# Optimization experiments

Measured on AMD Instinct MI355X. Metric: run time of the kernel, lower is better.

## Reference

```python
import jax, jax.numpy as jnp
import numpy as np

B, S, E, H = 64, 512, 768, 256


def setup_inputs() -> dict:
    key = jax.random.key(0)
    ks = jax.random.split(key, 9)
    sc = 0.02  # small init so relu-activated LSTM stays numerically sane
    x = jax.random.normal(ks[0], (B, S, E), dtype=jnp.float32)
    kernel_f = jax.random.normal(ks[1], (E, 4 * H), dtype=jnp.float32) * sc
    rec_f = jax.random.normal(ks[2], (H, 4 * H), dtype=jnp.float32) * sc
    bias_f = jnp.zeros((4 * H,), dtype=jnp.float32)
    kernel_b = jax.random.normal(ks[3], (E, 4 * H), dtype=jnp.float32) * sc
    rec_b = jax.random.normal(ks[4], (H, 4 * H), dtype=jnp.float32) * sc
    bias_b = jnp.zeros((4 * H,), dtype=jnp.float32)
    Wd = jax.random.normal(ks[5], (S * H, 2), dtype=jnp.float32) * sc
    bd = jnp.zeros((2,), dtype=jnp.float32)
    return {"x": x, "kernel_f": kernel_f, "rec_f": rec_f, "bias_f": bias_f,
            "kernel_b": kernel_b, "rec_b": rec_b, "bias_b": bias_b,
            "Wd": Wd, "bd": bd}


def _lstm_relu(x, kernel, rec, bias):
    # Keras LSTM with activation='relu', recurrent_activation='sigmoid'.
    # Gate order in keras kernel: [i, f, c, o].
    b, h = x.shape[0], rec.shape[0]
    xz = jnp.einsum('bse,eg->bsg', x, kernel) + bias  # [B,S,4H] precomputed input part

    def step(carry, zt):
        hp, cp = carry
        z = zt + hp @ rec  # [B,4H]
        zi, zf, zc, zo = jnp.split(z, 4, axis=-1)
        i = jax.nn.sigmoid(zi)
        f = jax.nn.sigmoid(zf)
        o = jax.nn.sigmoid(zo)
        c = f * cp + i * jax.nn.relu(zc)
        hn = o * jax.nn.relu(c)
        return (hn, c), hn

    init = (jnp.zeros((b, h), x.dtype), jnp.zeros((b, h), x.dtype))
    _, hs = jax.lax.scan(step, init, jnp.swapaxes(xz, 0, 1))  # [S,B,H]
    return jnp.swapaxes(hs, 0, 1)  # [B,S,H]


def reference(x, kernel_f, rec_f, bias_f, kernel_b, rec_b, bias_b, Wd, bd):
    h_fwd = _lstm_relu(x, kernel_f, rec_f, bias_f)
    # backward direction: process reversed sequence, reverse output back, then merge_mode='sum'
    h_bwd = _lstm_relu(x[:, ::-1], kernel_b, rec_b, bias_b)[:, ::-1]
    h = h_fwd + h_bwd  # [B,S,H]
    # dropout is identity at inference (training=None)
    flat = h.reshape(h.shape[0], -1)  # [B, S*H]
    logits = flat @ Wd + bd  # [B,2]
    return logits
```

## Files before the change

kernel.cpp:

```cpp
#include <hip/hip_runtime.h>
#include <hip/hip_bf16.h>
#include <hip/hip_fp16.h>

#define B_ 64
#define S_ 512
#define E_ 768
#define H_ 256
#define G_ 1024
#define MROWS 32768

typedef float f32x4 __attribute__((ext_vector_type(4)));
typedef float f32x16 __attribute__((ext_vector_type(16)));
typedef short short8 __attribute__((ext_vector_type(8)));
typedef _Float16 v2h __attribute__((ext_vector_type(2)));
typedef unsigned int u32x4 __attribute__((ext_vector_type(4)));


__global__ void cast_x_kernel(const float* __restrict__ x, __hip_bfloat16* __restrict__ xbf, int n) {
    int i = (blockIdx.x * 256 + threadIdx.x) * 4;
    if (i >= n) return;
    float4 v = *(const float4*)(x + i);
    xbf[i + 0] = __float2bfloat16(v.x);
    xbf[i + 1] = __float2bfloat16(v.y);
    xbf[i + 2] = __float2bfloat16(v.z);
    xbf[i + 3] = __float2bfloat16(v.w);
}

__global__ void prep_kT_kernel(const float* __restrict__ kf, const float* __restrict__ kb,
                               __hip_bfloat16* __restrict__ kT) {
    int idx = blockIdx.x * 256 + threadIdx.x;
    int dir = blockIdx.y;
    const float* src = dir ? kb : kf;
    int k = idx >> 10;
    int n = idx & 1023;
    float v = src[idx];
    kT[(size_t)dir * G_ * E_ + (size_t)n * E_ + k] = __float2bfloat16(v);
}

__global__ void prep_recQ_kernel(const float* __restrict__ rf, const float* __restrict__ rb,
                                 unsigned int* __restrict__ recQ) {
    int idx = blockIdx.x * 256 + threadIdx.x;
    int dir = blockIdx.y;
    const float* src = dir ? rb : rf;
    int g  = idx & 1023;
    int u  = (idx >> 10) & 3;
    int kk = idx >> 12;
    int k0 = 8 * kk + 2 * u;
    float a = src[(size_t)k0 * G_ + g];
    float b = src[(size_t)(k0 + 1) * G_ + g];
    v2h p;
    p[0] = (_Float16)a;
    p[1] = (_Float16)b;
    recQ[(size_t)dir * 131072 + (size_t)kk * 4096 + g * 4 + u] = __builtin_bit_cast(unsigned int, p);
}

#define TM 128
#define TN 128
#define BK 32
#define LDA 40

__global__ __launch_bounds__(256) void gemm_xz_kernel(
        const __hip_bfloat16* __restrict__ xbf,
        const __hip_bfloat16* __restrict__ kT,
        const float* __restrict__ bias_f, const float* __restrict__ bias_b,
        __hip_bfloat16* __restrict__ xz) {
    int dir  = blockIdx.z;
    int nblk = blockIdx.x;
    int mblk = blockIdx.y;
    int tid  = threadIdx.x;
    int wave = tid >> 6, lane = tid & 63;

    __shared__ __hip_bfloat16 shA[TM * LDA];
    __shared__ __hip_bfloat16 shB[TN * LDA];

    int m0 = mblk * TM;
    int n0 = nblk * TN;

    int rowl0 = tid >> 2;
    int rowl1 = rowl0 + 64;
    int k8    = (tid & 3) * 8;
    int ar0 = m0 + rowl0, ar1 = m0 + rowl1;
    int sa0 = (ar0 & ~511) | (dir ? (511 - (ar0 & 511)) : (ar0 & 511));
    int sa1 = (ar1 & ~511) | (dir ? (511 - (ar1 & 511)) : (ar1 & 511));
    const __hip_bfloat16* kbase = kT + (size_t)dir * G_ * E_;

    f32x16 acc[4] = {};

    int lm = lane & 31;
    int kq = (lane >> 5) * 8;

    for (int k0 = 0; k0 < E_; k0 += BK) {
        __syncthreads();
        *(short8*)&shA[rowl0 * LDA + k8] = *(const short8*)(xbf + (size_t)sa0 * E_ + k0 + k8);
        *(short8*)&shA[rowl1 * LDA + k8] = *(const short8*)(xbf + (size_t)sa1 * E_ + k0 + k8);
        *(short8*)&shB[rowl0 * LDA + k8] = *(const short8*)(kbase + (size_t)(n0 + rowl0) * E_ + k0 + k8);
        *(short8*)&shB[rowl1 * LDA + k8] = *(const short8*)(kbase + (size_t)(n0 + rowl1) * E_ + k0 + k8);
        __syncthreads();

#pragma unroll
        for (int kk = 0; kk < BK; kk += 16) {
            short8 afrag = *(const short8*)&shA[(wave * 32 + lm) * LDA + kk + kq];
#pragma unroll
            for (int j = 0; j < 4; ++j) {
                short8 bfrag = *(const short8*)&shB[(j * 32 + lm) * LDA + kk + kq];
                acc[j] = __builtin_amdgcn_mfma_f32_32x32x16_bf16(afrag, bfrag, acc[j], 0, 0, 0);
            }
        }
    }

    const float* bias = dir ? bias_b : bias_f;
#pragma unroll
    for (int j = 0; j < 4; ++j) {
        int col = n0 + j * 32 + lm;
        float bv = bias[col];
#pragma unroll
        for (int reg = 0; reg < 16; ++reg) {
            int row = m0 + wave * 32 + (reg & 3) + 8 * (reg >> 2) + 4 * (lane >> 5);
            xz[((size_t)dir * MROWS + row) * G_ + col] = __float2bfloat16(acc[j][reg] + bv);
        }
    }
}

__device__ inline float dot2f16(unsigned int rbits, unsigned int hbits, float acc) {
#if __has_builtin(__builtin_amdgcn_fdot2)
    return __builtin_amdgcn_fdot2(__builtin_bit_cast(v2h, rbits),
                                  __builtin_bit_cast(v2h, hbits), acc, false);
#else
    v2h r = __builtin_bit_cast(v2h, rbits);
    v2h h = __builtin_bit_cast(v2h, hbits);
    return acc + (float)r[0] * (float)h[0] + (float)r[1] * (float)h[1];
#endif
}

__device__ inline float sigmoidf(float x) { return 1.f / (1.f + __expf(-x)); }

#define KKREG 24
#define KKLDS 8
__global__ __launch_bounds__(512) void scan_kernel(
        const __hip_bfloat16* __restrict__ xz,
        const uint4* __restrict__ recQ,
        const float* __restrict__ Wd,
        const float* __restrict__ bd,
        float* __restrict__ out) {
    int b = blockIdx.x, dir = blockIdx.y, tid = threadIdx.x;
    __shared__ __align__(16) uint4 sh_rec[KKLDS * G_];
    __shared__ __align__(16) _Float16 sh_h[2][H_];
    __shared__ float sh_z[G_];
    __shared__ float rbuf[8];

    const uint4* rqbase = recQ + (size_t)dir * 32768;

    u32x4 rr0[KKREG], rr1[KKREG];
    {
        unsigned long long a0 = (unsigned long long)(const void*)(rqbase + tid);
        unsigned long long a1 = (unsigned long long)(const void*)(rqbase + tid + 512);
#pragma unroll
        for (int kk = 0; kk < KKREG; ++kk) {
            unsigned long long ka0 = a0 + (unsigned long long)kk * 16384ull;
            unsigned long long ka1 = a1 + (unsigned long long)kk * 16384ull;
            asm volatile("global_load_dwordx4 %0, %1, off" : "=v"(rr0[kk]) : "v"(ka0));
            asm volatile("global_load_dwordx4 %0, %1, off" : "=v"(rr1[kk]) : "v"(ka1));
        }
        asm volatile("s_waitcnt vmcnt(0)" ::: "memory");
    }

#pragma unroll
    for (int j = 0; j < KKLDS * 2; ++j)
        sh_rec[j * 512 + tid] = rqbase[KKREG * 1024 + j * 512 + tid];

    if (tid < H_) { sh_h[0][tid] = (_Float16)0.f; }
    float c = 0.f, pl0 = 0.f, pl1 = 0.f;
    const __hip_bfloat16* xzb = xz + ((size_t)dir * MROWS + (size_t)b * S_) * G_ + tid;
    __syncthreads();

    int p = 0;
    for (int s = 0; s < S_; ++s) {
        float xz0 = __bfloat162float(xzb[(size_t)s * G_]);
        float xz1 = __bfloat162float(xzb[(size_t)s * G_ + 512]);
        float2 wv = {0.f, 0.f};
        int t = dir ? (S_ - 1 - s) : s;
        if (tid < H_) wv = ((const float2*)Wd)[t * H_ + tid];

        const uint4* hp = (const uint4*)&sh_h[p][0];
        float z0a = 0.f, z0b = 0.f, z1a = 0.f, z1b = 0.f;

#pragma unroll
        for (int kk = 0; kk < KKREG; ++kk) {
            uint4 hv = hp[kk];
            u32x4 r0 = rr0[kk];
            u32x4 r1 = rr1[kk];
            z0a = dot2f16(r0.x, hv.x, z0a); z0b = dot2f16(r0.y, hv.y, z0b);
            z0a = dot2f16(r0.z, hv.z, z0a); z0b = dot2f16(r0.w, hv.w, z0b);
            z1a = dot2f16(r1.x, hv.x, z1a); z1b = dot2f16(r1.y, hv.y, z1b);
            z1a = dot2f16(r1.z, hv.z, z1a); z1b = dot2f16(r1.w, hv.w, z1b);
        }
#pragma unroll
        for (int j = 0; j < KKLDS; ++j) {
            uint4 hv = hp[KKREG + j];
            uint4 r0 = sh_rec[j * 1024 + tid];
            uint4 r1 = sh_rec[j * 1024 + tid + 512];
            z0a = dot2f16(r0.x, hv.x, z0a); z0b = dot2f16(r0.y, hv.y, z0b);
            z0a = dot2f16(r0.z, hv.z, z0a); z0b = dot2f16(r0.w, hv.w, z0b);
            z1a = dot2f16(r1.x, hv.x, z1a); z1b = dot2f16(r1.y, hv.y, z1b);
            z1a = dot2f16(r1.z, hv.z, z1a); z1b = dot2f16(r1.w, hv.w, z1b);
        }
        sh_z[tid]       = z0a + z0b + xz0;
        sh_z[tid + 512] = z1a + z1b + xz1;
        __syncthreads();

        if (tid < H_) {
            float zi = sh_z[tid];
            float zf = sh_z[H_ + tid];
            float zc = sh_z[2 * H_ + tid];
            float zo = sh_z[3 * H_ + tid];
            float ig = sigmoidf(zi);
            float fg = sigmoidf(zf);
            float og = sigmoidf(zo);
            float cc = fmaxf(zc, 0.f);
            c = fg * c + ig * cc;
            float h = og * fmaxf(c, 0.f);
            sh_h[p ^ 1][tid] = (_Float16)h;

            pl0 = fmaf(h, wv.x, pl0);
            pl1 = fmaf(h, wv.y, pl1);
        }
        __syncthreads();
        p ^= 1;
    }

    if (tid < H_) {
#pragma unroll
        for (int off = 32; off > 0; off >>= 1) {
            pl0 += __shfl_down(pl0, off);
            pl1 += __shfl_down(pl1, off);
        }
    }
    if (tid < H_ && (tid & 63) == 0) {
        int w = tid >> 6;
        rbuf[w] = pl0; rbuf[4 + w] = pl1;
    }
    __syncthreads();
    if (tid == 0) {
        float t0 = rbuf[0] + rbuf[1] + rbuf[2] + rbuf[3];
        float t1 = rbuf[4] + rbuf[5] + rbuf[6] + rbuf[7];
        atomicAdd(&out[b * 2 + 0], t0);
        atomicAdd(&out[b * 2 + 1], t1);
    }
    if (dir == 0 && tid < 2) atomicAdd(&out[b * 2 + tid], bd[tid]);
}

extern "C" void kernel_launch(void* const* d_in, const int* in_sizes, int n_in,
                              void* d_out, int out_size, void* d_ws, size_t ws_size,
                              hipStream_t stream) {
    const float* x        = (const float*)d_in[0];
    const float* kernel_f = (const float*)d_in[1];
    const float* rec_f    = (const float*)d_in[2];
    const float* bias_f   = (const float*)d_in[3];
    const float* kernel_b = (const float*)d_in[4];
    const float* rec_b    = (const float*)d_in[5];
    const float* bias_b   = (const float*)d_in[6];
    const float* Wd       = (const float*)d_in[7];
    const float* bd       = (const float*)d_in[8];
    float* out = (float*)d_out;

    char* w = (char*)d_ws;
    __hip_bfloat16* xz  = (__hip_bfloat16*)w;
    __hip_bfloat16* xbf = (__hip_bfloat16*)(w + 134217728);
    __hip_bfloat16* kT  = (__hip_bfloat16*)(w + 184549376);
    unsigned int*  recQ = (unsigned int*) (w + 187695104);

    int nx = B_ * S_ * E_;
    cast_x_kernel<<<nx / (256 * 4), 256, 0, stream>>>(x, xbf, nx);
    prep_kT_kernel<<<dim3((E_ * G_) / 256, 2), 256, 0, stream>>>(kernel_f, kernel_b, kT);
    prep_recQ_kernel<<<dim3(131072 / 256, 2), 256, 0, stream>>>(rec_f, rec_b, recQ);

    gemm_xz_kernel<<<dim3(G_ / TN, MROWS / TM, 2), 256, 0, stream>>>(xbf, kT, bias_f, bias_b, xz);

    hipMemsetAsync(d_out, 0, (size_t)out_size * sizeof(float), stream);
    scan_kernel<<<dim3(B_, 2), 512, 0, stream>>>(xz, (const uint4*)recQ, Wd, bd, out);
}
```

Baseline: 1.190 ms.

## Remap gate columns so each wavefront holds all four gates and drop one barrier

Threads are remapped so that a lane pair (lane, lane^32) computes all four gate pre-activations for one hidden unit. The gates are exchanged with a cross-lane shuffle instead of an LDS round trip, which removes the sh_z buffer and one __syncthreads per timestep. All 512 threads now run the gate math, half of them redundantly, with the projection contribution masked by wsel. The xz and Wd loads for the next step are also prefetched one iteration ahead to hide global latency on the serial recurrence.

```diff
diff --git a/kernel.cpp b/kernel.cpp
--- a/kernel.cpp
+++ b/kernel.cpp
@@ -145,15 +145,19 @@
     int b = blockIdx.x, dir = blockIdx.y, tid = threadIdx.x;
     __shared__ __align__(16) uint4 sh_rec[KKLDS * G_];
     __shared__ __align__(16) _Float16 sh_h[2][H_];
-    __shared__ float sh_z[G_];
-    __shared__ float rbuf[8];
+    __shared__ float rbuf[16];
+
+    int w = tid >> 6, lane = tid & 63, lm = lane & 31, hi = lane >> 5;
+    int col = w * 32 + lm;
+    int g0  = col + hi * 512;
+    int g1  = g0 + 256;
 
     const uint4* rqbase = recQ + (size_t)dir * 32768;
 
     u32x4 rr0[KKREG], rr1[KKREG];
     {
-        unsigned long long a0 = (unsigned long long)(const void*)(rqbase + tid);
-        unsigned long long a1 = (unsigned long long)(const void*)(rqbase + tid + 512);
+        unsigned long long a0 = (unsigned long long)(const void*)(rqbase + g0);
+        unsigned long long a1 = (unsigned long long)(const void*)(rqbase + g1);
 #pragma unroll
         for (int kk = 0; kk < KKREG; ++kk) {
             unsigned long long ka0 = a0 + (unsigned long long)kk * 16384ull;
@@ -168,18 +172,27 @@
     for (int j = 0; j < KKLDS * 2; ++j)
         sh_rec[j * 512 + tid] = rqbase[KKREG * 1024 + j * 512 + tid];
 
-    if (tid < H_) { sh_h[0][tid] = (_Float16)0.f; }
+    if (tid < H_) sh_h[0][tid] = (_Float16)0.f;
     float c = 0.f, pl0 = 0.f, pl1 = 0.f;
-    const __hip_bfloat16* xzb = xz + ((size_t)dir * MROWS + (size_t)b * S_) * G_ + tid;
+    float wsel = hi ? 0.f : 1.f;
+    const __hip_bfloat16* xrb = xz + ((size_t)dir * MROWS + (size_t)b * S_) * G_;
     __syncthreads();
+
+    float nxz0 = __bfloat162float(xrb[g0]);
+    float nxz1 = __bfloat162float(xrb[g1]);
+    int t0i = dir ? (S_ - 1) : 0;
+    float2 nwv = ((const float2*)Wd)[t0i * H_ + col];
 
     int p = 0;
     for (int s = 0; s < S_; ++s) {
-        float xz0 = __bfloat162float(xzb[(size_t)s * G_]);
-        float xz1 = __bfloat162float(xzb[(size_t)s * G_ + 512]);
-        float2 wv = {0.f, 0.f};
-        int t = dir ? (S_ - 1 - s) : s;
-        if (tid < H_) wv = ((const float2*)Wd)[t * H_ + tid];
+        float xz0 = nxz0, xz1 = nxz1;
+        float2 wv = nwv;
+
+        int sn = (s + 1 < S_) ? (s + 1) : (S_ - 1);
+        int tn = dir ? (S_ - 1 - sn) : sn;
+        nxz0 = __bfloat162float(xrb[(size_t)sn * G_ + g0]);
+        nxz1 = __bfloat162float(xrb[(size_t)sn * G_ + g1]);
+        nwv  = ((const float2*)Wd)[tn * H_ + col];
 
         const uint4* hp = (const uint4*)&sh_h[p][0];
         float z0a = 0.f, z0b = 0.f, z1a = 0.f, z1b = 0.f;
@@ -197,52 +210,52 @@
 #pragma unroll
         for (int j = 0; j < KKLDS; ++j) {
             uint4 hv = hp[KKREG + j];
-            uint4 r0 = sh_rec[j * 1024 + tid];
-            uint4 r1 = sh_rec[j * 1024 + tid + 512];
+            uint4 r0 = sh_rec[j * 1024 + g0];
+            uint4 r1 = sh_rec[j * 1024 + g1];
             z0a = dot2f16(r0.x, hv.x, z0a); z0b = dot2f16(r0.y, hv.y, z0b);
             z0a = dot2f16(r0.z, hv.z, z0a); z0b = dot2f16(r0.w, hv.w, z0b);
             z1a = dot2f16(r1.x, hv.x, z1a); z1b = dot2f16(r1.y, hv.y, z1b);
             z1a = dot2f16(r1.z, hv.z, z1a); z1b = dot2f16(r1.w, hv.w, z1b);
         }
-        sh_z[tid]       = z0a + z0b + xz0;
-        sh_z[tid + 512] = z1a + z1b + xz1;
-        __syncthreads();
-
-        if (tid < H_) {
-            float zi = sh_z[tid];
-            float zf = sh_z[H_ + tid];
-            float zc = sh_z[2 * H_ + tid];
-            float zo = sh_z[3 * H_ + tid];
-            float ig = sigmoidf(zi);
-            float fg = sigmoidf(zf);
-            float og = sigmoidf(zo);
-            float cc = fmaxf(zc, 0.f);
-            c = fg * c + ig * cc;
-            float h = og * fmaxf(c, 0.f);
-            sh_h[p ^ 1][tid] = (_Float16)h;
-
-            pl0 = fmaf(h, wv.x, pl0);
-            pl1 = fmaf(h, wv.y, pl1);
-        }
+
+        float z0 = z0a + z0b + xz0;
+        float z1 = z1a + z1b + xz1;
+
+        float zx0 = __shfl_xor(z0, 32);
+        float zx1 = __shfl_xor(z1, 32);
+        float zi = hi ? zx0 : z0;
+        float zf = hi ? zx1 : z1;
+        float zc = hi ? z0 : zx0;
+        float zo = hi ? z1 : zx1;
+
+        float ig = sigmoidf(zi);
+        float fg = sigmoidf(zf);
+        float og = sigmoidf(zo);
+        float cc = fmaxf(zc, 0.f);
+        c = fg * c + ig * cc;
+        float h = og * fmaxf(c, 0.f);
+        if (hi == 0) sh_h[p ^ 1][col] = (_Float16)h;
+
+        pl0 = fmaf(h, wv.x * wsel, pl0);
+        pl1 = fmaf(h, wv.y * wsel, pl1);
+
         __syncthreads();
         p ^= 1;
     }
 
-    if (tid < H_) {
-#pragma unroll
-        for (int off = 32; off > 0; off >>= 1) {
-            pl0 += __shfl_down(pl0, off);
-            pl1 += __shfl_down(pl1, off);
-        }
-    }
-    if (tid < H_ && (tid & 63) == 0) {
-        int w = tid >> 6;
-        rbuf[w] = pl0; rbuf[4 + w] = pl1;
+#pragma unroll
+    for (int off = 32; off > 0; off >>= 1) {
+        pl0 += __shfl_down(pl0, off);
+        pl1 += __shfl_down(pl1, off);
+    }
+    if (lane == 0) {
+        rbuf[w] = pl0; rbuf[8 + w] = pl1;
     }
     __syncthreads();
     if (tid == 0) {
-        float t0 = rbuf[0] + rbuf[1] + rbuf[2] + rbuf[3];
-        float t1 = rbuf[4] + rbuf[5] + rbuf[6] + rbuf[7];
+        float t0 = 0.f, t1 = 0.f;
+#pragma unroll
+        for (int i = 0; i < 8; ++i) { t0 += rbuf[i]; t1 += rbuf[8 + i]; }
         atomicAdd(&out[b * 2 + 0], t0);
         atomicAdd(&out[b * 2 + 1], t1);
     }
```

Measured after the change: 1.145 ms. 1.04x faster.

## Batch LSTM scan across 16 sequences with MFMA and split hidden units across workgroup pairs

Applied to the files above, without the earlier changes.

The recurrent scan no longer runs one workgroup per (batch, direction) doing per-thread fp16 dot2 products. It now runs 16 workgroups. Each handles 16 batch rows and half of the hidden units, and computes the recurrent matmul with 16x16x32 f16 MFMA, using weights pre-swizzled into register-resident fragments. The two halves of each pair exchange h every step through a global buffer and a spin-wait on atomic counters. The next step's xz values are prefetched and the gate math runs directly on the accumulators. The aim is to replace scalar dot-product work with matrix instructions and fit all weights in registers, at the cost of a global handshake on every timestep and far fewer workgroups.

```diff
diff --git a/kernel.cpp b/kernel.cpp
--- a/kernel.cpp
+++ b/kernel.cpp
@@ -13,6 +13,7 @@
 typedef float f32x16 __attribute__((ext_vector_type(16)));
 typedef short short8 __attribute__((ext_vector_type(8)));
 typedef _Float16 v2h __attribute__((ext_vector_type(2)));
+typedef _Float16 h8 __attribute__((ext_vector_type(8)));
 typedef unsigned int u32x4 __attribute__((ext_vector_type(4)));
 
 
@@ -37,21 +38,26 @@
     kT[(size_t)dir * G_ * E_ + (size_t)n * E_ + k] = __float2bfloat16(v);
 }
 
-__global__ void prep_recQ_kernel(const float* __restrict__ rf, const float* __restrict__ rb,
-                                 unsigned int* __restrict__ recQ) {
+__global__ void prep_recF_kernel(const float* __restrict__ rf_, const float* __restrict__ rb_,
+                                 uint4* __restrict__ recF) {
     int idx = blockIdx.x * 256 + threadIdx.x;
-    int dir = blockIdx.y;
-    const float* src = dir ? rb : rf;
-    int g  = idx & 1023;
-    int u  = (idx >> 10) & 3;
-    int kk = idx >> 12;
-    int k0 = 8 * kk + 2 * u;
-    float a = src[(size_t)k0 * G_ + g];
-    float b = src[(size_t)(k0 + 1) * G_ + g];
-    v2h p;
-    p[0] = (_Float16)a;
-    p[1] = (_Float16)b;
-    recQ[(size_t)dir * 131072 + (size_t)kk * 4096 + g * 4 + u] = __builtin_bit_cast(unsigned int, p);
+    int dir = idx >> 15;
+    const float* src = dir ? rb_ : rf_;
+    int li   = idx & 63;
+    int ks   = (idx >> 6) & 7;
+    int tile = (idx >> 9) & 63;
+    int gc = tile * 16 + (li & 15);
+    int k0 = ks * 32 + (li >> 4) * 8;
+    unsigned int wds[4];
+#pragma unroll
+    for (int u = 0; u < 4; ++u) {
+        _Float16 a  = (_Float16)src[(size_t)(k0 + 2 * u) * G_ + gc];
+        _Float16 b2 = (_Float16)src[(size_t)(k0 + 2 * u + 1) * G_ + gc];
+        wds[u] = (unsigned int)__builtin_bit_cast(unsigned short, a) |
+                 ((unsigned int)__builtin_bit_cast(unsigned short, b2) << 16);
+    }
+    uint4 q; q.x = wds[0]; q.y = wds[1]; q.z = wds[2]; q.w = wds[3];
+    recF[idx] = q;
 }
 
 #define TM 128
@@ -121,132 +127,151 @@
     }
 }
 
-__device__ inline float dot2f16(unsigned int rbits, unsigned int hbits, float acc) {
-#if __has_builtin(__builtin_amdgcn_fdot2)
-    return __builtin_amdgcn_fdot2(__builtin_bit_cast(v2h, rbits),
-                                  __builtin_bit_cast(v2h, hbits), acc, false);
-#else
-    v2h r = __builtin_bit_cast(v2h, rbits);
-    v2h h = __builtin_bit_cast(v2h, hbits);
-    return acc + (float)r[0] * (float)h[0] + (float)r[1] * (float)h[1];
-#endif
-}
-
 __device__ inline float sigmoidf(float x) { return 1.f / (1.f + __expf(-x)); }
-
-#define KKREG 24
-#define KKLDS 8
-__global__ __launch_bounds__(512) void scan_kernel(
+__device__ inline float bfu(unsigned int u) { return __builtin_bit_cast(float, u << 16); }
+
+__global__ __launch_bounds__(512, 2) void scan_kernel(
         const __hip_bfloat16* __restrict__ xz,
-        const uint4* __restrict__ recQ,
+        const uint4* __restrict__ recF,
         const float* __restrict__ Wd,
         const float* __restrict__ bd,
+        int* __restrict__ ctr,
+        uint4* __restrict__ hx,
         float* __restrict__ out) {
-    int b = blockIdx.x, dir = blockIdx.y, tid = threadIdx.x;
-    __shared__ __align__(16) uint4 sh_rec[KKLDS * G_];
-    __shared__ __align__(16) _Float16 sh_h[2][H_];
-    __shared__ float sh_z[G_];
-    __shared__ float rbuf[8];
-
-    const uint4* rqbase = recQ + (size_t)dir * 32768;
-
-    u32x4 rr0[KKREG], rr1[KKREG];
+    int wg = blockIdx.x;
+    int pair = wg & 7, half = wg >> 3;
+    int bg = pair & 3, dir = pair >> 2;
+    int tid = threadIdx.x;
+    int w = tid >> 6, l = tid & 63, l15 = l & 15, l4 = l >> 4;
+
+    __shared__ uint4 HlU[2][512];
+    __shared__ float rbuf[8][16][2];
+
+    int hbase = half * 128 + w * 16;
+    int gb = hbase + l4 * 4;
+
+    u32x4 rr[4][8];
     {
-        unsigned long long a0 = (unsigned long long)(const void*)(rqbase + tid);
-        unsigned long long a1 = (unsigned long long)(const void*)(rqbase + tid + 512);
-#pragma unroll
-        for (int kk = 0; kk < KKREG; ++kk) {
-            unsigned long long ka0 = a0 + (unsigned long long)kk * 16384ull;
-            unsigned long long ka1 = a1 + (unsigned long long)kk * 16384ull;
-            asm volatile("global_load_dwordx4 %0, %1, off" : "=v"(rr0[kk]) : "v"(ka0));
-            asm volatile("global_load_dwordx4 %0, %1, off" : "=v"(rr1[kk]) : "v"(ka1));
-        }
+        const uint4* rbase = recF + (size_t)dir * 32768 + (size_t)(half * 8 + w) * 8 * 64 + l;
+        unsigned long long a0 = (unsigned long long)(const void*)rbase;
+#pragma unroll
+        for (int r = 0; r < 4; ++r)
+#pragma unroll
+            for (int ks = 0; ks < 8; ++ks) {
+                unsigned long long ka = a0 + (unsigned long long)(r * 131072 + ks * 1024);
+                asm volatile("global_load_dwordx4 %0, %1, off" : "=v"(rr[r][ks]) : "v"(ka));
+            }
         asm volatile("s_waitcnt vmcnt(0)" ::: "memory");
     }
 
-#pragma unroll
-    for (int j = 0; j < KKLDS * 2; ++j)
-        sh_rec[j * 512 + tid] = rqbase[KKREG * 1024 + j * 512 + tid];
-
-    if (tid < H_) { sh_h[0][tid] = (_Float16)0.f; }
-    float c = 0.f, pl0 = 0.f, pl1 = 0.f;
-    const __hip_bfloat16* xzb = xz + ((size_t)dir * MROWS + (size_t)b * S_) * G_ + tid;
+    HlU[0][tid] = make_uint4(0u, 0u, 0u, 0u);
+
+    const __hip_bfloat16* xzb = xz + ((size_t)dir * MROWS + (size_t)(bg * 16 + l15) * S_) * G_;
+
+    uint2 nx[4];
+#pragma unroll
+    for (int r = 0; r < 4; ++r)
+        nx[r] = *(const uint2*)(xzb + (r * 256 + gb));
+
+    int* cme = ctr + pair * 2 + half;
+    int* cot = ctr + pair * 2 + (half ^ 1);
+    uint4* hxp = hx + (size_t)pair * 1024;
+
+    int eks = half * 4 + (w >> 1);
+    int ekq = (w & 1) * 2 + (l4 >> 1);
+    int eidx16 = ((eks * 4 + ekq) * 16 + l15) * 8 + (l4 & 1) * 4;
+
+    f32x4 c_ = {0.f, 0.f, 0.f, 0.f};
+    float pl0 = 0.f, pl1 = 0.f;
     __syncthreads();
 
     int p = 0;
     for (int s = 0; s < S_; ++s) {
-        float xz0 = __bfloat162float(xzb[(size_t)s * G_]);
-        float xz1 = __bfloat162float(xzb[(size_t)s * G_ + 512]);
-        float2 wv = {0.f, 0.f};
-        int t = dir ? (S_ - 1 - s) : s;
-        if (tid < H_) wv = ((const float2*)Wd)[t * H_ + tid];
-
-        const uint4* hp = (const uint4*)&sh_h[p][0];
-        float z0a = 0.f, z0b = 0.f, z1a = 0.f, z1b = 0.f;
-
-#pragma unroll
-        for (int kk = 0; kk < KKREG; ++kk) {
-            uint4 hv = hp[kk];
-            u32x4 r0 = rr0[kk];
-            u32x4 r1 = rr1[kk];
-            z0a = dot2f16(r0.x, hv.x, z0a); z0b = dot2f16(r0.y, hv.y, z0b);
-            z0a = dot2f16(r0.z, hv.z, z0a); z0b = dot2f16(r0.w, hv.w, z0b);
-            z1a = dot2f16(r1.x, hv.x, z1a); z1b = dot2f16(r1.y, hv.y, z1b);
-            z1a = dot2f16(r1.z, hv.z, z1a); z1b = dot2f16(r1.w, hv.w, z1b);
-        }
-#pragma unroll
-        for (int j = 0; j < KKLDS; ++j) {
-            uint4 hv = hp[KKREG + j];
-            uint4 r0 = sh_rec[j * 1024 + tid];
-            uint4 r1 = sh_rec[j * 1024 + tid + 512];
-            z0a = dot2f16(r0.x, hv.x, z0a); z0b = dot2f16(r0.y, hv.y, z0b);
-            z0a = dot2f16(r0.z, hv.z, z0a); z0b = dot2f16(r0.w, hv.w, z0b);
-            z1a = dot2f16(r1.x, hv.x, z1a); z1b = dot2f16(r1.y, hv.y, z1b);
-            z1a = dot2f16(r1.z, hv.z, z1a); z1b = dot2f16(r1.w, hv.w, z1b);
-        }
-        sh_z[tid]       = z0a + z0b + xz0;
-        sh_z[tid + 512] = z1a + z1b + xz1;
-        __syncthreads();
-
-        if (tid < H_) {
-            float zi = sh_z[tid];
-            float zf = sh_z[H_ + tid];
-            float zc = sh_z[2 * H_ + tid];
-            float zo = sh_z[3 * H_ + tid];
-            float ig = sigmoidf(zi);
-            float fg = sigmoidf(zf);
-            float og = sigmoidf(zo);
-            float cc = fmaxf(zc, 0.f);
-            c = fg * c + ig * cc;
-            float h = og * fmaxf(c, 0.f);
-            sh_h[p ^ 1][tid] = (_Float16)h;
-
-            pl0 = fmaf(h, wv.x, pl0);
-            pl1 = fmaf(h, wv.y, pl1);
-        }
-        __syncthreads();
-        p ^= 1;
-    }
-
-    if (tid < H_) {
-#pragma unroll
-        for (int off = 32; off > 0; off >>= 1) {
-            pl0 += __shfl_down(pl0, off);
-            pl1 += __shfl_down(pl1, off);
-        }
-    }
-    if (tid < H_ && (tid & 63) == 0) {
-        int w = tid >> 6;
-        rbuf[w] = pl0; rbuf[4 + w] = pl1;
-    }
+        int tt = dir ? (S_ - 1 - s) : s;
+
+        f32x4 acc[4];
+#pragma unroll
+        for (int r = 0; r < 4; ++r) {
+            uint2 v = nx[r];
+            f32x4 a;
+            a[0] = bfu(v.x & 0xffffu); a[1] = bfu(v.x >> 16);
+            a[2] = bfu(v.y & 0xffffu); a[3] = bfu(v.y >> 16);
+            acc[r] = a;
+        }
+        int sn = (s + 1 < S_) ? (s + 1) : (S_ - 1);
+#pragma unroll
+        for (int r = 0; r < 4; ++r)
+            nx[r] = *(const uint2*)(xzb + (size_t)sn * G_ + (r * 256 + gb));
+
+        const float* wdp = Wd + (size_t)(tt * 256 + gb) * 2;
+        float4 w0 = *(const float4*)(wdp);
+        float4 w1 = *(const float4*)(wdp + 4);
+
+        const uint4* hb = &HlU[p][0];
+#pragma unroll
+        for (int ks = 0; ks < 8; ++ks) {
+            h8 hf = __builtin_bit_cast(h8, hb[ks * 64 + l4 * 16 + l15]);
+#pragma unroll
+            for (int r = 0; r < 4; ++r)
+                acc[r] = __builtin_amdgcn_mfma_f32_16x16x32_f16(
+                    __builtin_bit_cast(h8, rr[r][ks]), hf, acc[r], 0, 0, 0);
+        }
+
+        f32x4 hh;
+#pragma unroll
+        for (int e = 0; e < 4; ++e) {
+            float ig = sigmoidf(acc[0][e]);
+            float fg = sigmoidf(acc[1][e]);
+            float og = sigmoidf(acc[3][e]);
+            float cand = fmaxf(acc[2][e], 0.f);
+            float cn = fg * c_[e] + ig * cand;
+            c_[e] = cn;
+            hh[e] = og * fmaxf(cn, 0.f);
+        }
+        pl0 += hh[0] * w0.x + hh[1] * w0.z + hh[2] * w1.x + hh[3] * w1.z;
+        pl1 += hh[0] * w0.y + hh[1] * w0.w + hh[2] * w1.y + hh[3] * w1.w;
+
+        if (s < S_ - 1) {
+            unsigned int lo = (unsigned int)__builtin_bit_cast(unsigned short, (_Float16)hh[0]) |
+                              ((unsigned int)__builtin_bit_cast(unsigned short, (_Float16)hh[1]) << 16);
+            unsigned int hi2 = (unsigned int)__builtin_bit_cast(unsigned short, (_Float16)hh[2]) |
+                               ((unsigned int)__builtin_bit_cast(unsigned short, (_Float16)hh[3]) << 16);
+            uint2 st; st.x = lo; st.y = hi2;
+            *(uint2*)((char*)&HlU[p ^ 1][0] + eidx16 * 2) = st;
+            *(uint2*)((char*)(hxp + (size_t)(s & 1) * 512) + eidx16 * 2) = st;
+
+            __syncthreads();
+            if (tid == 0) {
+                __threadfence();
+                __hip_atomic_fetch_add(cme, 1, __ATOMIC_RELAXED, __HIP_MEMORY_SCOPE_AGENT);
+                while (__hip_atomic_load(cot, __ATOMIC_RELAXED, __HIP_MEMORY_SCOPE_AGENT) <= s)
+                    __builtin_amdgcn_s_sleep(1);
+                __threadfence();
+            }
+            __syncthreads();
+            int ph = half ^ 1;
+            if (tid < 256)
+                HlU[p ^ 1][ph * 256 + tid] = hxp[(size_t)(s & 1) * 512 + ph * 256 + tid];
+            __syncthreads();
+            p ^= 1;
+        }
+    }
+
+#pragma unroll
+    for (int off = 16; off <= 32; off <<= 1) {
+        pl0 += __shfl_xor(pl0, off);
+        pl1 += __shfl_xor(pl1, off);
+    }
+    if (l < 16) { rbuf[w][l][0] = pl0; rbuf[w][l][1] = pl1; }
     __syncthreads();
-    if (tid == 0) {
-        float t0 = rbuf[0] + rbuf[1] + rbuf[2] + rbuf[3];
-        float t1 = rbuf[4] + rbuf[5] + rbuf[6] + rbuf[7];
-        atomicAdd(&out[b * 2 + 0], t0);
-        atomicAdd(&out[b * 2 + 1], t1);
-    }
-    if (dir == 0 && tid < 2) atomicAdd(&out[b * 2 + tid], bd[tid]);
+    if (tid < 16) {
+        float t0 = 0.f, t1 = 0.f;
+#pragma unroll
+        for (int ww = 0; ww < 8; ++ww) { t0 += rbuf[ww][tid][0]; t1 += rbuf[ww][tid][1]; }
+        if (dir == 0 && half == 0) { t0 += bd[0]; t1 += bd[1]; }
+        atomicAdd(&out[(bg * 16 + tid) * 2 + 0], t0);
+        atomicAdd(&out[(bg * 16 + tid) * 2 + 1], t1);
+    }
 }
 
 extern "C" void kernel_launch(void* const* d_in, const int* in_sizes, int n_in,
@@ -267,15 +292,18 @@
     __hip_bfloat16* xz  = (__hip_bfloat16*)w;
     __hip_bfloat16* xbf = (__hip_bfloat16*)(w + 134217728);
     __hip_bfloat16* kT  = (__hip_bfloat16*)(w + 184549376);
-    unsigned int*  recQ = (unsigned int*) (w + 187695104);
+    uint4*         recF = (uint4*)        (w + 187695104);
+    uint4* hx  = (uint4*)(w + 134217728);
+    int*   ctr = (int*)  (w + 134217728 + 131072);
 
     int nx = B_ * S_ * E_;
     cast_x_kernel<<<nx / (256 * 4), 256, 0, stream>>>(x, xbf, nx);
     prep_kT_kernel<<<dim3((E_ * G_) / 256, 2), 256, 0, stream>>>(kernel_f, kernel_b, kT);
-    prep_recQ_kernel<<<dim3(131072 / 256, 2), 256, 0, stream>>>(rec_f, rec_b, recQ);
+    prep_recF_kernel<<<256, 256, 0, stream>>>(rec_f, rec_b, recF);
 
     gemm_xz_kernel<<<dim3(G_ / TN, MROWS / TM, 2), 256, 0, stream>>>(xbf, kT, bias_f, bias_b, xz);
 
     hipMemsetAsync(d_out, 0, (size_t)out_size * sizeof(float), stream);
-    scan_kernel<<<dim3(B_, 2), 512, 0, stream>>>(xz, (const uint4*)recQ, Wd, bd, out);
-}
+    hipMemsetAsync(ctr, 0, 64, stream);
+    scan_kernel<<<dim3(16), 512, 0, stream>>>(xz, recF, Wd, bd, ctr, hx, out);
+}
```

Measured after the change: 1.820 ms. 53.0% more time.
